# Performance work log

Measured on AMD Instinct MI355X. Metric: run time of the kernel, lower is better.

Reference implementation:

```python
import jax, jax.numpy as jnp
import numpy as np

NBATCH, NATOM, NEIGH = 16, 512, 64
NTYPE, NWAVE, NIPSIN, NORBIT = 4, 8, 3, 128
CUTOFF = 5.0
NPAIR = NATOM * NEIGH  # neighbor pairs per configuration


def _make_index_para(nipsin):
    # [0, 1,1,1, 2,...(9 times)] -> angular-order label per channel
    parts = [np.zeros(1, np.int32)]
    for i in range(1, nipsin):
        parts.append(np.full(3 ** i, i, np.int32))
    return jnp.asarray(np.concatenate(parts))


def setup_inputs() -> dict:
    key = jax.random.key(0)
    ks = jax.random.split(key, 10)
    cart = jax.random.uniform(ks[0], (NBATCH, NATOM, 3), jnp.float32) * 6.0
    numatoms = jnp.full((NBATCH,), NATOM, dtype=jnp.int32)
    species = jax.random.randint(ks[1], (NBATCH * NATOM,), 0, NTYPE).astype(jnp.int32)
    atom_index = jax.random.randint(ks[2], (2, NBATCH, NPAIR), 0, NATOM).astype(jnp.int32)
    shifts = jnp.zeros((NBATCH, NPAIR, 3), jnp.float32)  # all pairs valid (pass >-1e10 check)
    # learned parameters / buffers
    rs = jnp.tile(jnp.linspace(0.5, 4.0, NWAVE, dtype=jnp.float32)[None, :], (NTYPE, 1))
    inta = -(jax.random.uniform(ks[3], (NTYPE, NWAVE), jnp.float32) * 0.9 + 0.1)
    params = jnp.ones((NTYPE, NWAVE), jnp.float32) / float(NEIGH)
    hyper = jax.random.normal(ks[4], (1, NIPSIN, NWAVE, NORBIT), jnp.float32) * (1.0 / np.sqrt(NWAVE))
    index_para = _make_index_para(NIPSIN)
    return {"cart": cart, "numatoms": numatoms, "species": species,
            "atom_index": atom_index, "shifts": shifts,
            "rs": rs, "inta": inta, "params": params, "hyper": hyper,
            "index_para": index_para, "cutoff": CUTOFF}


def _angular(dist_vec, f_cut, nipsin):
    # dist_vec: [N,3], f_cut: [N] -> [L, N] with L = 1 + 3 + ... + 3^(nipsin-1)
    dv = dist_vec.T  # [3, N]
    orb = f_cut[None, :]
    parts = [orb]
    for _ in range(1, nipsin):
        orb = (orb[:, None, :] * dv[None, :, :]).reshape(-1, dv.shape[1])
        parts.append(orb)
    return jnp.concatenate(parts, axis=0)


def reference(cart, numatoms, species, atom_index, shifts, rs, inta, params, hyper, index_para, cutoff):
    nbatch, natom, _ = cart.shape
    totnatom = nbatch * natom
    cart_ = cart.reshape(totnatom, 3)
    # offset per-config neighbor indices to global atom ids
    offs = (jnp.arange(nbatch, dtype=atom_index.dtype) * natom)[None, :, None]
    idx12 = (atom_index + offs).reshape(2, -1)  # [2, Npairs]
    dist_vec = cart_[idx12[0]] - cart_[idx12[1]] + shifts.reshape(-1, 3)  # [Npairs,3]
    distances = jnp.linalg.norm(dist_vec, axis=-1)  # [Npairs]
    sp_j = species[idx12[1]]
    f_cut = jnp.square(0.5 * jnp.cos(distances * (jnp.pi / cutoff)) + 0.5)
    # per-pair gaussian radial basis, gathered by neighbor element type
    radial = jnp.exp(inta[sp_j] * jnp.square(distances[:, None] - rs[sp_j]))  # [Npairs, nwave]
    ang = _angular(dist_vec, f_cut, NIPSIN)  # [L, Npairs]
    orbital = ang.T[:, :, None] * radial[:, None, :]  # [Npairs, L, nwave]
    orb_coeff = params[species]  # [totnatom, nwave] (all species >= 0)
    # iteration 0 (ocmod_list is empty, so no refinement loop)
    worb = orbital * orb_coeff[idx12[1]][:, None, :]  # [Npairs, L, nwave]
    sum_worb = jax.ops.segment_sum(worb, idx12[0], num_segments=totnatom)  # [totnatom, L, nwave]
    hp = hyper[0][index_para]  # [L, nwave, norbit]
    hw = jnp.einsum('ijk,jkm->ijm', sum_worb, hp)  # [totnatom, L, norbit]
    density = jnp.sum(jnp.square(hw), axis=1)  # [totnatom, norbit]
    return density
```

## Files before the change

kernel.cpp:

```cpp
#include <hip/hip_runtime.h>
#include <hip/hip_bf16.h>

#define NBATCH  16
#define NATOM   512
#define NEIGH   64
#define NPAIR   (NATOM * NEIGH)
#define TOTPAIR (NBATCH * NPAIR)
#define TOTATOM (NBATCH * NATOM)
#define NTYPE   4
#define NWAVE   8
#define NL      13
#define NORBIT  128
#define CAP     128
#define CAPP    130
#define NSUB    8
#define SUBCAP  40
#define PAIRS_PER_SUB (NPAIR / NSUB)


__global__ __launch_bounds__(512) void fill_kernel(
    const int* __restrict__ atom_index,
    int*       __restrict__ count,
    unsigned short* __restrict__ bucket)
{
    const int b   = blockIdx.x >> 3;
    const int s   = blockIdx.x & 7;
    const int tid = threadIdx.x;

    __shared__ int s_cnt[NATOM];
    s_cnt[tid] = 0;
    __syncthreads();

#pragma unroll
    for (int it = 0; it < PAIRS_PER_SUB / 512; ++it) {
        int pl = s * PAIRS_PER_SUB + it * 512 + tid;
        int il = atom_index[b * NPAIR + pl];
        int slot = atomicAdd(&s_cnt[il], 1);
        if (slot < SUBCAP)
            bucket[((size_t)((b * NATOM + il) * NSUB + s)) * SUBCAP + slot] =
                (unsigned short)pl;
    }
    __syncthreads();

    count[(b * NATOM + tid) * NSUB + s] = s_cnt[tid];
}

__global__ __launch_bounds__(128) void gather_kernel(
    const float* __restrict__ cart,
    const int*   __restrict__ species,
    const int*   __restrict__ atom_index,
    const float* __restrict__ shifts,
    const float* __restrict__ rs,
    const float* __restrict__ inta,
    const float* __restrict__ params,
    const float* __restrict__ cutoff_p,
    const int*   __restrict__ count,
    const unsigned short* __restrict__ bucket,
    const float* __restrict__ hyper,
    float*       __restrict__ out)
{
    const int i    = blockIdx.x;
    const int b    = i >> 9;
    const int base = b << 9;
    const int tid  = threadIdx.x;

    __shared__ float s_a [NL][CAPP];
    __shared__ float s_rp[NWAVE][CAPP];
    __shared__ float s_S [NL * NWAVE];
    __shared__ float s_tab[3 * NTYPE * NWAVE];
    __shared__ int   s_off[NSUB + 1];

    if (tid < NTYPE * NWAVE) {
        s_tab[tid]                     = rs[tid];
        s_tab[NTYPE * NWAVE + tid]     = inta[tid];
        s_tab[2 * NTYPE * NWAVE + tid] = params[tid];
    }
    if (tid == 0) {
        int o = 0;
#pragma unroll
        for (int s2 = 0; s2 < NSUB; ++s2) {
            s_off[s2] = o;
            int c = count[i * NSUB + s2];
            o += (c < SUBCAP ? c : SUBCAP);
        }
        s_off[NSUB] = o;
    }
    __syncthreads();

    int total = s_off[NSUB];
    if (total > CAP) total = CAP;

    const float cx  = cart[3 * i + 0];
    const float cy  = cart[3 * i + 1];
    const float cz  = cart[3 * i + 2];
    const float pic = 3.14159265358979323846f / cutoff_p[0];

    for (int k = tid; k < total; k += 128) {
        int s2 = 0;
#pragma unroll
        for (int t = 1; t < NSUB; ++t)
            if (k >= s_off[t]) s2 = t;
        int local = k - s_off[s2];
        int pl = (int)bucket[((size_t)(i * NSUB + s2)) * SUBCAP + local];
        int p  = (b << 15) | pl;
        int j  = atom_index[TOTPAIR + p] + base;

        float dx = cx - cart[3 * j + 0] + shifts[3 * p + 0];
        float dy = cy - cart[3 * j + 1] + shifts[3 * p + 1];
        float dz = cz - cart[3 * j + 2] + shifts[3 * p + 2];
        float d  = sqrtf(dx * dx + dy * dy + dz * dz);

        float c  = 0.5f * __cosf(d * pic) + 0.5f;
        float fc = c * c;

        float a1 = fc * dx, a2 = fc * dy, a3 = fc * dz;
        s_a[0][k]  = fc;
        s_a[1][k]  = a1;       s_a[2][k]  = a2;       s_a[3][k]  = a3;
        s_a[4][k]  = a1 * dx;  s_a[5][k]  = a1 * dy;  s_a[6][k]  = a1 * dz;
        s_a[7][k]  = a2 * dx;  s_a[8][k]  = a2 * dy;  s_a[9][k]  = a2 * dz;
        s_a[10][k] = a3 * dx;  s_a[11][k] = a3 * dy;  s_a[12][k] = a3 * dz;

        int sp = species[j];
#pragma unroll
        for (int w = 0; w < NWAVE; ++w) {
            float tt = d - s_tab[sp * NWAVE + w];
            s_rp[w][k] = __expf(s_tab[NTYPE * NWAVE + sp * NWAVE + w] * tt * tt)
                       * s_tab[2 * NTYPE * NWAVE + sp * NWAVE + w];
        }
    }
    __syncthreads();

    if (tid < NL * NWAVE) {
        int l = tid >> 3, w = tid & 7;
        float S = 0.0f;
        int k = 0;
        for (; k + 1 < total; k += 2) {
            float2 av = *(const float2*)&s_a[l][k];
            float2 rv = *(const float2*)&s_rp[w][k];
            S += av.x * rv.x;
            S += av.y * rv.y;
        }
        if (k < total) S += s_a[l][k] * s_rp[w][k];
        s_S[tid] = S;
    }
    __syncthreads();

    const int m = tid;
    float acc = 0.0f;
#pragma unroll
    for (int l = 0; l < NL; ++l) {
        int ip = (l == 0) ? 0 : ((l < 4) ? 1 : 2);
        const float* hp = hyper + (size_t)ip * (NWAVE * NORBIT) + m;
        float h = 0.0f;
#pragma unroll
        for (int w = 0; w < NWAVE; ++w)
            h += s_S[l * NWAVE + w] * hp[w * NORBIT];
        acc += h * h;
    }
    out[(size_t)i * NORBIT + m] = acc;
}

extern "C" void kernel_launch(void* const* d_in, const int* in_sizes, int n_in,
                              void* d_out, int out_size, void* d_ws, size_t ws_size,
                              hipStream_t stream) {
    const float* cart       = (const float*)d_in[0];
    const int*   species    = (const int*)  d_in[2];
    const int*   atom_index = (const int*)  d_in[3];
    const float* shifts     = (const float*)d_in[4];
    const float* rs         = (const float*)d_in[5];
    const float* inta       = (const float*)d_in[6];
    const float* params     = (const float*)d_in[7];
    const float* hyper      = (const float*)d_in[8];
    const float* cutoff_p   = (const float*)d_in[10];

    int* count = (int*)d_ws;
    unsigned short* bucket =
        (unsigned short*)((char*)d_ws + (size_t)TOTATOM * NSUB * sizeof(int));
    float* out = (float*)d_out;

    fill_kernel<<<NBATCH * NSUB, 512, 0, stream>>>(atom_index, count, bucket);

    gather_kernel<<<TOTATOM, 128, 0, stream>>>(
        cart, species, atom_index, shifts, rs, inta, params, cutoff_p,
        count, bucket, hyper, out);
}
```

Measured before the change: 109.0 us.

## Precompute pair displacement and species in fill kernel, store float4 buckets

The fill kernel now stages the batch's coordinates and species in shared memory. It computes each pair's displacement vector and neighbor species there and writes them as a float4 record into the bucket instead of a 16-bit pair index. The gather kernel reads one contiguous float4 per pair, removing its dependent random loads of atom_index, cart, shifts and species. In exchange, bucket storage and write traffic grow eightfold, and the fill kernel does more loads and arithmetic.

```diff
diff --git a/kernel.cpp b/kernel.cpp
--- a/kernel.cpp
+++ b/kernel.cpp
@@ -1,5 +1,4 @@
 #include <hip/hip_runtime.h>
-#include <hip/hip_bf16.h>
 
 #define NBATCH  16
 #define NATOM   512
@@ -19,26 +18,45 @@
 
 
 __global__ __launch_bounds__(512) void fill_kernel(
-    const int* __restrict__ atom_index,
-    int*       __restrict__ count,
-    unsigned short* __restrict__ bucket)
+    const float* __restrict__ cart,
+    const int*   __restrict__ species,
+    const int*   __restrict__ atom_index,
+    const float* __restrict__ shifts,
+    int*         __restrict__ count,
+    float4*      __restrict__ bucket)
 {
     const int b   = blockIdx.x >> 3;
     const int s   = blockIdx.x & 7;
     const int tid = threadIdx.x;
 
-    __shared__ int s_cnt[NATOM];
+    __shared__ float s_cart[NATOM * 3];
+    __shared__ int   s_spc [NATOM];
+    __shared__ int   s_cnt [NATOM];
+
+    s_cart[tid]        = cart[b * NATOM * 3 + tid];
+    s_cart[tid + 512]  = cart[b * NATOM * 3 + tid + 512];
+    s_cart[tid + 1024] = cart[b * NATOM * 3 + tid + 1024];
+    s_spc[tid] = species[b * NATOM + tid];
     s_cnt[tid] = 0;
     __syncthreads();
 
 #pragma unroll
     for (int it = 0; it < PAIRS_PER_SUB / 512; ++it) {
         int pl = s * PAIRS_PER_SUB + it * 512 + tid;
-        int il = atom_index[b * NPAIR + pl];
+        int p  = b * NPAIR + pl;
+        int il = atom_index[p];
+        int jl = atom_index[TOTPAIR + p];
+
+        float dx = s_cart[3 * il + 0] - s_cart[3 * jl + 0] + shifts[3 * p + 0];
+        float dy = s_cart[3 * il + 1] - s_cart[3 * jl + 1] + shifts[3 * p + 1];
+        float dz = s_cart[3 * il + 2] - s_cart[3 * jl + 2] + shifts[3 * p + 2];
+        int   sp = s_spc[jl];
+
         int slot = atomicAdd(&s_cnt[il], 1);
-        if (slot < SUBCAP)
+        if (slot < SUBCAP) {
             bucket[((size_t)((b * NATOM + il) * NSUB + s)) * SUBCAP + slot] =
-                (unsigned short)pl;
+                make_float4(dx, dy, dz, __int_as_float(sp));
+        }
     }
     __syncthreads();
 
@@ -46,23 +64,17 @@
 }
 
 __global__ __launch_bounds__(128) void gather_kernel(
-    const float* __restrict__ cart,
-    const int*   __restrict__ species,
-    const int*   __restrict__ atom_index,
-    const float* __restrict__ shifts,
     const float* __restrict__ rs,
     const float* __restrict__ inta,
     const float* __restrict__ params,
     const float* __restrict__ cutoff_p,
     const int*   __restrict__ count,
-    const unsigned short* __restrict__ bucket,
+    const float4* __restrict__ bucket,
     const float* __restrict__ hyper,
     float*       __restrict__ out)
 {
-    const int i    = blockIdx.x;
-    const int b    = i >> 9;
-    const int base = b << 9;
-    const int tid  = threadIdx.x;
+    const int i   = blockIdx.x;
+    const int tid = threadIdx.x;
 
     __shared__ float s_a [NL][CAPP];
     __shared__ float s_rp[NWAVE][CAPP];
@@ -90,9 +102,6 @@
     int total = s_off[NSUB];
     if (total > CAP) total = CAP;
 
-    const float cx  = cart[3 * i + 0];
-    const float cy  = cart[3 * i + 1];
-    const float cz  = cart[3 * i + 2];
     const float pic = 3.14159265358979323846f / cutoff_p[0];
 
     for (int k = tid; k < total; k += 128) {
@@ -101,13 +110,10 @@
         for (int t = 1; t < NSUB; ++t)
             if (k >= s_off[t]) s2 = t;
         int local = k - s_off[s2];
-        int pl = (int)bucket[((size_t)(i * NSUB + s2)) * SUBCAP + local];
-        int p  = (b << 15) | pl;
-        int j  = atom_index[TOTPAIR + p] + base;
+        float4 rec = bucket[((size_t)(i * NSUB + s2)) * SUBCAP + local];
 
-        float dx = cx - cart[3 * j + 0] + shifts[3 * p + 0];
-        float dy = cy - cart[3 * j + 1] + shifts[3 * p + 1];
-        float dz = cz - cart[3 * j + 2] + shifts[3 * p + 2];
+        float dx = rec.x, dy = rec.y, dz = rec.z;
+        int   sp = __float_as_int(rec.w);
         float d  = sqrtf(dx * dx + dy * dy + dz * dz);
 
         float c  = 0.5f * __cosf(d * pic) + 0.5f;
@@ -120,7 +126,6 @@
         s_a[7][k]  = a2 * dx;  s_a[8][k]  = a2 * dy;  s_a[9][k]  = a2 * dz;
         s_a[10][k] = a3 * dx;  s_a[11][k] = a3 * dy;  s_a[12][k] = a3 * dz;
 
-        int sp = species[j];
 #pragma unroll
         for (int w = 0; w < NWAVE; ++w) {
             float tt = d - s_tab[sp * NWAVE + w];
@@ -174,13 +179,14 @@
     const float* cutoff_p   = (const float*)d_in[10];
 
     int* count = (int*)d_ws;
-    unsigned short* bucket =
-        (unsigned short*)((char*)d_ws + (size_t)TOTATOM * NSUB * sizeof(int));
+    float4* bucket =
+        (float4*)((char*)d_ws + (size_t)TOTATOM * NSUB * sizeof(int));
+
     float* out = (float*)d_out;
 
-    fill_kernel<<<NBATCH * NSUB, 512, 0, stream>>>(atom_index, count, bucket);
+    fill_kernel<<<NBATCH * NSUB, 512, 0, stream>>>(
+        cart, species, atom_index, shifts, count, bucket);
 
     gather_kernel<<<TOTATOM, 128, 0, stream>>>(
-        cart, species, atom_index, shifts, rs, inta, params, cutoff_p,
-        count, bucket, hyper, out);
+        rs, inta, params, cutoff_p, count, bucket, hyper, out);
 }
```

New measurement: 109.9 us. About the same (+0.8%).
